# Optimization experiments

Measured on AMD Instinct MI355X. Metric: run time of the kernel, lower is better.

Reference implementation:

```python
import jax, jax.numpy as jnp
import numpy as np
import math

# ---- static config (mirrors init_kwargs) ----
B, CIN, COUT = 8, 32, 32
H, W = 256, 256
RADIUS_CUTOFF = 0.03
NR, NPHI = 6, 7               # kernel_shape = [6, 7] (anisotropic basis)
K = (NR - 1) * NPHI + 1       # 36 basis functions
EPS = 1e-5                    # InstanceNorm2d eps
NEG_SLOPE = 0.2


def _disco_psi(nh, nw, r_cutoff, nr, nphi):
    """Local DISCO filter basis on an equidistant [-1,1]^2 grid.
    Returns psi [K, P, P] (float32) and half-width p (P = 2p+1).
    Piecewise-linear hat functions in radius (nr rings incl. center) times
    hat functions in angle (nphi sectors), normalized and quadrature-weighted."""
    dy = 2.0 / nh
    dx = 2.0 / nw
    p = int(math.floor(r_cutoff / min(dx, dy)))
    off_y = (np.arange(-p, p + 1) * dy)[:, None]
    off_x = (np.arange(-p, p + 1) * dx)[None, :]
    r = np.sqrt(off_x ** 2 + off_y ** 2)                 # [P, P]
    phi = np.arctan2(off_y + 0 * off_x, off_x + 0 * off_y) % (2.0 * np.pi)
    dr = r_cutoff / nr
    dphi = 2.0 * np.pi / nphi
    ker = (nr - 1) * nphi + 1
    ik = np.arange(ker)[:, None, None]                   # [K,1,1]
    ir = ((ik - 1) // nphi + 1) * dr                     # ik=0 -> ring at r=0
    iphi = ((ik - 1) % nphi) * dphi
    norm = np.pi * (r_cutoff * nr / (nr + 1)) ** 2       # 2d normalization
    rv = np.clip(1.0 - np.abs(r[None] - ir) / dr, 0.0, None) * (r[None] <= r_cutoff)
    dphi_abs = np.abs(phi[None] - iphi)
    dphi_min = np.minimum(dphi_abs, 2.0 * np.pi - dphi_abs)
    pv = np.where(ik > 0, np.clip(1.0 - dphi_min / dphi, 0.0, None), 1.0)
    q = dx * dy                                          # quadrature weight
    psi = (rv * pv) * (q / norm)
    return jnp.asarray(psi, jnp.float32), p


def _upsample2x_bilinear_align_corners(x):
    """torch nn.Upsample(scale_factor=2, mode='bilinear', align_corners=True)."""
    b, c, hi, wi = x.shape
    ho, wo = 2 * hi, 2 * wi
    ys = jnp.linspace(0.0, hi - 1.0, ho)
    y0 = jnp.clip(jnp.floor(ys), 0, hi - 2).astype(jnp.int32)
    wy = (ys - y0.astype(ys.dtype))[None, None, :, None]
    x = x[:, :, y0, :] * (1.0 - wy) + x[:, :, y0 + 1, :] * wy
    xs = jnp.linspace(0.0, wi - 1.0, wo)
    x0 = jnp.clip(jnp.floor(xs), 0, wi - 2).astype(jnp.int32)
    wx = (xs - x0.astype(xs.dtype))[None, None, None, :]
    return x[:, :, :, x0] * (1.0 - wx) + x[:, :, :, x0 + 1] * wx


def setup_inputs() -> dict:
    key = jax.random.key(0)
    k1, k2 = jax.random.split(key)
    image = jax.random.normal(k1, (B, CIN, H, W), dtype=jnp.float32)
    # DISCO learnable weights: [out_ch, in_ch, kernel_size]
    scale = 1.0 / np.sqrt(CIN * K)
    weight = jax.random.normal(k2, (COUT, CIN, K), dtype=jnp.float32) * scale
    return {"image": image, "weight": weight}


def reference(image, weight):
    x = _upsample2x_bilinear_align_corners(image)
    # 2) equidistant DISCO conv: assemble dense kernel from basis, strided conv back to (H,W)
    psi, p = _disco_psi(2 * H, 2 * W, RADIUS_CUTOFF / 2.0, NR, NPHI)   # [K,P,P]
    kernel = jnp.einsum("oik,kyx->oiyx", weight, psi)                   # [O,I,P,P]
    y = jax.lax.conv_general_dilated(
        x, kernel, window_strides=(2, 2), padding=[(p, p), (p, p)],
        dimension_numbers=("NCHW", "OIHW", "NCHW"))                     # [B,O,H,W]
    # 3) InstanceNorm2d (no affine), biased variance over spatial dims
    mean = jnp.mean(y, axis=(2, 3), keepdims=True)
    var = jnp.var(y, axis=(2, 3), keepdims=True)
    y = (y - mean) * jax.lax.rsqrt(var + EPS)
    # 4) LeakyReLU(0.2)
    return jnp.where(y >= 0, y, NEG_SLOPE * y)
```

## Files before the change

kernel.cpp:

```cpp
#include <hip/hip_runtime.h>
#include <hip/hip_bf16.h>
#include <math.h>

#define B_     8
#define CIN_   32
#define COUT_  32
#define H_     256
#define W_     256
#define K_     36
#define P_     3
#define KW_    7
#define TAPS_  49
#define EPS_   1e-5f
#define SLOPE_ 0.2f

#define PART_OFF_F   28672
#define MEANRS_OFF_F 159744

#define IMG_PLANE_B   6736
#define IMG_ROW_B     336

#define XP_ROW   304
#define XO_BASE  11248

using short8_t  = __attribute__((ext_vector_type(8)))  short;
using f32x16_t  = __attribute__((ext_vector_type(16))) float;
using f32x4_t   = __attribute__((ext_vector_type(4)))  float;

__device__ inline ushort f32_to_bf16(float f) {
    unsigned int bits = __float_as_uint(f);
    unsigned int r = (bits + 0x7FFFu + ((bits >> 16) & 1u)) >> 16;
    return (ushort)r;
}

__global__ __launch_bounds__(256)
void build_kernel(const float* __restrict__ weight, ushort* __restrict__ kerB) {
    __shared__ float psi_s[2][K_];
    const int f  = blockIdx.x;
    const int p  = f & 3;
    const int ky = (f >> 2) % 7;
    const int oc = f / 28;
    const int tid = threadIdx.x;

    if (tid < 2 * K_) {
        const int tt = tid / K_;
        const int k  = tid - tt * K_;
        const int kx = 2 * p + tt;
        float val = 0.f;
        if (kx <= 6) {
            const double dxy   = 2.0 / 512.0;
            const double rcut  = 0.015;
            const int    nr    = 6, nphi = 7;
            const double dr    = rcut / nr;
            const double dphi  = 2.0 * M_PI / nphi;
            const double norm  = M_PI * (rcut * nr / (nr + 1)) * (rcut * nr / (nr + 1));
            const double q     = dxy * dxy;
            const double offy = (double)(ky - P_) * dxy;
            const double offx = (double)(kx - P_) * dxy;
            const double r    = sqrt(offx * offx + offy * offy);
            double phi = atan2(offy, offx);
            if (phi < 0.0) phi += 2.0 * M_PI;
            double ir, iphi;
            if (k == 0) { ir = 0.0; iphi = 0.0; }
            else        { ir = (double)((k - 1) / nphi + 1) * dr;
                          iphi = (double)((k - 1) % nphi) * dphi; }
            double rv = 1.0 - fabs(r - ir) / dr;
            rv = rv > 0.0 ? rv : 0.0;
            if (r > rcut) rv = 0.0;
            double pv = 1.0;
            if (k > 0) {
                double da = fabs(phi - iphi);
                double dm = da < (2.0 * M_PI - da) ? da : (2.0 * M_PI - da);
                pv = 1.0 - dm / dphi;
                pv = pv > 0.0 ? pv : 0.0;
            }
            val = (float)(rv * pv * q / norm);
        }
        psi_s[tt][k] = val;
    }
    __syncthreads();

    for (int e = tid; e < 512; e += 256) {
        const int lane = e >> 3;
        const int j    = e & 7;
        const int gs   = lane >> 5;
        const int n    = lane & 31;
        const int kx   = 2 * p + gs;
        float s = 0.f;
        if (kx <= 6) {
            const int ci = oc * 8 + j;
            const float* w = weight + (size_t)(n * CIN_ + ci) * K_;
            #pragma unroll
            for (int k = 0; k < K_; ++k) s = fmaf(w[k], psi_s[gs][k], s);
        }
        kerB[((size_t)f * 64 + lane) * 8 + j] = f32_to_bf16(s);
    }
}

__global__ __launch_bounds__(512, 8)
void conv_mfma(const float* __restrict__ image,
               const ushort* __restrict__ kerB,
               float* __restrict__ out,
               float* __restrict__ partials) {
    __shared__ float  Img_s[3368];
    __shared__ ushort Xup_s[11248];
    __shared__ float  wp[8][32][2];

    const int tid  = threadIdx.x;
    const int lane = tid & 63;
    const int w    = tid >> 6;
    const int j0 = blockIdx.x * 16;
    const int i0 = blockIdx.y * 16;
    const int b  = blockIdx.z;

    const int u0 = 2 * i0 - 3;
    const int v0 = 2 * j0 - 3;
    const int R0 = i0 - 2;
    const int C0 = j0 - 2;

    const int gs  = lane >> 5;
    const int tio = (lane & 31) >> 4;
    const int tj  = lane & 15;
    const int yb0 = 4 * w + 2 * tio;

    f32x16_t acc;
    #pragma unroll
    for (int q = 0; q < 16; ++q) acc[q] = 0.f;

    char* img_bytes = (char*)Img_s;
    char* xup_bytes = (char*)Xup_s;

    const float* imgb = image + (size_t)(b * CIN_) * (H_ * W_);

    for (int oc = 0; oc < 4; ++oc) {
        const float* img = imgb + (size_t)(oc * 8) * (H_ * W_);
        for (int e = tid; e < 800; e += 512) {
            const int p  = (e >= 400) ? 1 : 0;
            const int yx = e - p * 400;
            const int py = yx / 20, px = yx - py * 20;
            const int row = R0 + py, col = C0 + px;
            f32x4_t g = {0.f, 0.f, 0.f, 0.f};
            if ((unsigned)row < 256u && (unsigned)col < 256u) {
                const float* q = img + (size_t)p * 4 * (H_ * W_) + row * W_ + col;
                g[0] = q[0];
                g[1] = q[H_ * W_];
                g[2] = q[2 * (H_ * W_)];
                g[3] = q[3 * (H_ * W_)];
            }
            *(f32x4_t*)(img_bytes + p * IMG_PLANE_B + (py * 21 + px) * 16) = g;
        }
        __syncthreads();

        for (int e = tid; e < 703; e += 512) {
            const int y   = e / 19;
            const int xp  = e - 19 * y;
            const int x   = 2 * xp;
            const int ry  = y >> 1;
            const float wy =
                (float)((((y & 1) ? 510 : 255)) - (R0 + ry)) * (1.0f / 511.0f);
            const int Ax = C0 + xp;
            const float wx0 = (float)(255 - Ax) * (1.0f / 511.0f);
            const float wx1 = (float)(510 - Ax) * (1.0f / 511.0f);
            const bool oky = ((unsigned)(u0 + y) < 512u);
            const bool ok0 = oky && ((unsigned)(v0 + x) < 512u);
            const bool ok1 = oky && ((unsigned)(v0 + x + 1) < 512u) && (xp < 18);

            const char* lo = img_bytes + (ry * 21 + xp) * 16;
            const char* hi = lo + IMG_PLANE_B;
            const f32x4_t a00 = *(const f32x4_t*)(lo);
            const f32x4_t a01 = *(const f32x4_t*)(lo + 16);
            const f32x4_t a10 = *(const f32x4_t*)(lo + IMG_ROW_B);
            const f32x4_t a11 = *(const f32x4_t*)(lo + IMG_ROW_B + 16);
            const f32x4_t b00 = *(const f32x4_t*)(hi);
            const f32x4_t b01 = *(const f32x4_t*)(hi + 16);
            const f32x4_t b10 = *(const f32x4_t*)(hi + IMG_ROW_B);
            const f32x4_t b11 = *(const f32x4_t*)(hi + IMG_ROW_B + 16);

            const f32x4_t cA0 = a00 + wy * (a10 - a00);
            const f32x4_t cA1 = a01 + wy * (a11 - a01);
            const f32x4_t cB0 = b00 + wy * (b10 - b00);
            const f32x4_t cB1 = b01 + wy * (b11 - b01);

            {
                const f32x4_t va = cA0 + wx0 * (cA1 - cA0);
                const f32x4_t vb = cB0 + wx0 * (cB1 - cB0);
                __hip_bfloat162 h0 = __float22bfloat162_rn(make_float2(va[0], va[1]));
                __hip_bfloat162 h1 = __float22bfloat162_rn(make_float2(va[2], va[3]));
                __hip_bfloat162 h2 = __float22bfloat162_rn(make_float2(vb[0], vb[1]));
                __hip_bfloat162 h3 = __float22bfloat162_rn(make_float2(vb[2], vb[3]));
                union { short8_t s8; uint4 u4; } pk;
                pk.u4.x = ok0 ? *(unsigned int*)&h0 : 0u;
                pk.u4.y = ok0 ? *(unsigned int*)&h1 : 0u;
                pk.u4.z = ok0 ? *(unsigned int*)&h2 : 0u;
                pk.u4.w = ok0 ? *(unsigned int*)&h3 : 0u;
                *(short8_t*)(xup_bytes + y * XP_ROW + xp * 16) = pk.s8;
            }
            {
                const f32x4_t va = cA0 + wx1 * (cA1 - cA0);
                const f32x4_t vb = cB0 + wx1 * (cB1 - cB0);
                __hip_bfloat162 h0 = __float22bfloat162_rn(make_float2(va[0], va[1]));
                __hip_bfloat162 h1 = __float22bfloat162_rn(make_float2(va[2], va[3]));
                __hip_bfloat162 h2 = __float22bfloat162_rn(make_float2(vb[0], vb[1]));
                __hip_bfloat162 h3 = __float22bfloat162_rn(make_float2(vb[2], vb[3]));
                union { short8_t s8; uint4 u4; } pk;
                pk.u4.x = ok1 ? *(unsigned int*)&h0 : 0u;
                pk.u4.y = ok1 ? *(unsigned int*)&h1 : 0u;
                pk.u4.z = ok1 ? *(unsigned int*)&h2 : 0u;
                pk.u4.w = ok1 ? *(unsigned int*)&h3 : 0u;
                *(short8_t*)(xup_bytes + XO_BASE + y * XP_ROW + xp * 16) = pk.s8;
            }
        }
        __syncthreads();

        const int pbase = (gs ? XO_BASE : 0) + tj * 16;
        const ushort* kbp = kerB + ((size_t)(oc * 28) * 64 + lane) * 8;
        #pragma unroll
        for (int ky = 0; ky < KW_; ++ky) {
            short8_t bf[4];
            #pragma unroll
            for (int p = 0; p < 4; ++p)
                bf[p] = *(const short8_t*)(kbp + (size_t)(ky * 4 + p) * 512);
            const int rbase = pbase + (yb0 + ky) * XP_ROW;
            #pragma unroll
            for (int p = 0; p < 4; ++p) {
                const short8_t afrag = *(const short8_t*)(xup_bytes + rbase + p * 16);
                acc = __builtin_amdgcn_mfma_f32_32x32x16_bf16(afrag, bf[p], acc, 0, 0, 0);
            }
        }
        __syncthreads();
    }

    const int n = lane & 31;
    float* op = out + (size_t)(b * COUT_ + n) * (H_ * W_);
    const int ibase = i0 + 2 * w;
    #pragma unroll
    for (int grp = 0; grp < 4; ++grp) {
        const int ti  = ibase + (grp >> 1);
        const int tjj = j0 + ((grp & 1) ? 8 : 0) + 4 * gs;
        f32x4_t s;
        s[0] = acc[grp * 4 + 0]; s[1] = acc[grp * 4 + 1];
        s[2] = acc[grp * 4 + 2]; s[3] = acc[grp * 4 + 3];
        *(f32x4_t*)(op + (size_t)ti * W_ + tjj) = s;
    }

    float s1 = 0.f, s2 = 0.f;
    #pragma unroll
    for (int q = 0; q < 16; ++q) { s1 += acc[q]; s2 = fmaf(acc[q], acc[q], s2); }
    s1 += __shfl_xor(s1, 32);
    s2 += __shfl_xor(s2, 32);
    if (lane < 32) { wp[w][lane][0] = s1; wp[w][lane][1] = s2; }
    __syncthreads();
    if (tid < 32) {
        float t1 = 0.f, t2 = 0.f;
        #pragma unroll
        for (int wv = 0; wv < 8; ++wv) { t1 += wp[wv][tid][0]; t2 += wp[wv][tid][1]; }
        const int tile = blockIdx.y * 16 + blockIdx.x;
        float2* pp = (float2*)partials;
        pp[((b * 32 + tid) << 8) | tile] = make_float2(t1, t2);
    }
}

__global__ __launch_bounds__(64)
void stats_kernel(const float* __restrict__ partials, float* __restrict__ meanrs) {
    const int bo = blockIdx.x;
    const int l  = threadIdx.x;
    const float2* pp = (const float2*)partials + ((size_t)bo << 8);
    float s1 = 0.f, s2 = 0.f;
    #pragma unroll
    for (int k = 0; k < 4; ++k) {
        const float2 p = pp[l + 64 * k];
        s1 += p.x; s2 += p.y;
    }
    #pragma unroll
    for (int off = 32; off > 0; off >>= 1) {
        s1 += __shfl_down(s1, off);
        s2 += __shfl_down(s2, off);
    }
    if (l == 0) {
        const float inv = 1.0f / 65536.0f;
        const float m   = s1 * inv;
        const float var = s2 * inv - m * m;
        ((float2*)meanrs)[bo] = make_float2(m, 1.0f / sqrtf(var + EPS_));
    }
}

__global__ __launch_bounds__(256)
void norm2_kernel(float* __restrict__ y, const float* __restrict__ meanrs) {
    const int blk = blockIdx.x;
    const int bo  = blk >> 6;
    const float2 mr = ((const float2*)meanrs)[bo];
    const float m  = mr.x;
    const float rs = mr.y;

    const int e = blk * 256 + threadIdx.x;
    float4 v = ((const float4*)y)[e];
    v.x = (v.x - m) * rs; v.x = v.x >= 0.f ? v.x : SLOPE_ * v.x;
    v.y = (v.y - m) * rs; v.y = v.y >= 0.f ? v.y : SLOPE_ * v.y;
    v.z = (v.z - m) * rs; v.z = v.z >= 0.f ? v.z : SLOPE_ * v.z;
    v.w = (v.w - m) * rs; v.w = v.w >= 0.f ? v.w : SLOPE_ * v.w;
    ((float4*)y)[e] = v;
}

extern "C" void kernel_launch(void* const* d_in, const int* in_sizes, int n_in,
                              void* d_out, int out_size, void* d_ws, size_t ws_size,
                              hipStream_t stream) {
    const float* image  = (const float*)d_in[0];
    const float* weight = (const float*)d_in[1];
    float*  out      = (float*)d_out;
    ushort* kerB     = (ushort*)d_ws;
    float*  partials = (float*)d_ws + PART_OFF_F;
    float*  meanrs   = (float*)d_ws + MEANRS_OFF_F;

    build_kernel<<<dim3(112), dim3(256), 0, stream>>>(weight, kerB);
    conv_mfma<<<dim3(16, 16, B_), dim3(512), 0, stream>>>(image, kerB, out, partials);
    stats_kernel<<<dim3(256), dim3(64), 0, stream>>>(partials, meanrs);
    norm2_kernel<<<dim3(16384), dim3(256), 0, stream>>>(out, meanrs);
}
```

Baseline: 122.6 us.

## Pack conv taps in flat pairs to cut padded MFMA work

The 49 filter taps are now grouped into 25 flat tap pairs instead of 7 rows of 4 column pairs, where each row had one zero-padded slot. This lowers the MFMA count per channel group from 28 to 25. The weight-packing kernel and the A-fragment addressing are changed to match, and the LDS row pitch is widened so each pair's fragment can be addressed across rows, with a special case for the final half-empty pair. The cost is a larger shared-memory footprint, which may reduce occupancy, plus more complex address arithmetic.

```diff
diff --git a/kernel.cpp b/kernel.cpp
--- a/kernel.cpp
+++ b/kernel.cpp
@@ -11,17 +11,18 @@
 #define P_     3
 #define KW_    7
 #define TAPS_  49
+#define NPAIR_ 25
 #define EPS_   1e-5f
 #define SLOPE_ 0.2f
 
-#define PART_OFF_F   28672
-#define MEANRS_OFF_F 159744
+#define PART_OFF_F   25600
+#define MEANRS_OFF_F 156672
 
 #define IMG_PLANE_B   6736
 #define IMG_ROW_B     336
 
-#define XP_ROW   304
-#define XO_BASE  11248
+#define XP_ROW   336
+#define XO_BASE  12480
 
 using short8_t  = __attribute__((ext_vector_type(8)))  short;
 using f32x16_t  = __attribute__((ext_vector_type(16))) float;
@@ -37,17 +38,18 @@
 void build_kernel(const float* __restrict__ weight, ushort* __restrict__ kerB) {
     __shared__ float psi_s[2][K_];
     const int f  = blockIdx.x;
-    const int p  = f & 3;
-    const int ky = (f >> 2) % 7;
-    const int oc = f / 28;
+    const int i  = f % NPAIR_;
+    const int oc = f / NPAIR_;
     const int tid = threadIdx.x;
 
     if (tid < 2 * K_) {
         const int tt = tid / K_;
         const int k  = tid - tt * K_;
-        const int kx = 2 * p + tt;
+        const int tap = 2 * i + tt;
         float val = 0.f;
-        if (kx <= 6) {
+        if (tap <= 48) {
+            const int ky = tap / 7;
+            const int kx = tap % 7;
             const double dxy   = 2.0 / 512.0;
             const double rcut  = 0.015;
             const int    nr    = 6, nphi = 7;
@@ -85,9 +87,9 @@
         const int j    = e & 7;
         const int gs   = lane >> 5;
         const int n    = lane & 31;
-        const int kx   = 2 * p + gs;
+        const int tap  = 2 * i + gs;
         float s = 0.f;
-        if (kx <= 6) {
+        if (tap <= 48) {
             const int ci = oc * 8 + j;
             const float* w = weight + (size_t)(n * CIN_ + ci) * K_;
             #pragma unroll
@@ -103,7 +105,7 @@
                float* __restrict__ out,
                float* __restrict__ partials) {
     __shared__ float  Img_s[3368];
-    __shared__ ushort Xup_s[11248];
+    __shared__ ushort Xup_s[12456];
     __shared__ float  wp[8][32][2];
 
     const int tid  = threadIdx.x;
@@ -212,19 +214,32 @@
         }
         __syncthreads();
 
-        const int pbase = (gs ? XO_BASE : 0) + tj * 16;
-        const ushort* kbp = kerB + ((size_t)(oc * 28) * 64 + lane) * 8;
+        const int abase = yb0 * XP_ROW + tj * 16;
+        const ushort* kbp = kerB + ((size_t)(oc * NPAIR_) * 64 + lane) * 8;
+        short8_t bf[5];
         #pragma unroll
-        for (int ky = 0; ky < KW_; ++ky) {
-            short8_t bf[4];
+        for (int gq = 0; gq < 5; ++gq) {
             #pragma unroll
-            for (int p = 0; p < 4; ++p)
-                bf[p] = *(const short8_t*)(kbp + (size_t)(ky * 4 + p) * 512);
-            const int rbase = pbase + (yb0 + ky) * XP_ROW;
+            for (int u = 0; u < 5; ++u)
+                bf[u] = *(const short8_t*)(kbp + (size_t)((gq * 5 + u) * 512));
             #pragma unroll
-            for (int p = 0; p < 4; ++p) {
-                const short8_t afrag = *(const short8_t*)(xup_bytes + rbase + p * 16);
-                acc = __builtin_amdgcn_mfma_f32_32x32x16_bf16(afrag, bf[p], acc, 0, 0, 0);
+            for (int u = 0; u < 5; ++u) {
+                const int i = gq * 5 + u;
+                int addr;
+                if (i < 24) {
+                    const int t0 = 2 * i, t1 = 2 * i + 1;
+                    const int c0 = (t0 / 7) * XP_ROW + ((t0 % 7) & 1 ? XO_BASE : 0)
+                                 + ((t0 % 7) >> 1) * 16;
+                    const int c1 = (t1 / 7) * XP_ROW + ((t1 % 7) & 1 ? XO_BASE : 0)
+                                 + ((t1 % 7) >> 1) * 16;
+                    addr = abase + (gs ? c1 : c0);
+                } else {
+                    const int c0 = 6 * XP_ROW + 3 * 16;
+                    addr = gs ? (XO_BASE + yb0 * XP_ROW + 18 * 16)
+                              : (abase + c0);
+                }
+                const short8_t afrag = *(const short8_t*)(xup_bytes + addr);
+                acc = __builtin_amdgcn_mfma_f32_32x32x16_bf16(afrag, bf[u], acc, 0, 0, 0);
             }
         }
         __syncthreads();
@@ -311,7 +326,7 @@
     float*  partials = (float*)d_ws + PART_OFF_F;
     float*  meanrs   = (float*)d_ws + MEANRS_OFF_F;
 
-    build_kernel<<<dim3(112), dim3(256), 0, stream>>>(weight, kerB);
+    build_kernel<<<dim3(4 * NPAIR_), dim3(256), 0, stream>>>(weight, kerB);
     conv_mfma<<<dim3(16, 16, B_), dim3(512), 0, stream>>>(image, kerB, out, partials);
     stats_kernel<<<dim3(256), dim3(64), 0, stream>>>(partials, meanrs);
     norm2_kernel<<<dim3(16384), dim3(256), 0, stream>>>(out, meanrs);
```

Result: slower. 158.3 us (+29.1%).

## Repack 7x7 conv taps into 25 bf16 MFMA pairs to drop padded taps

Applied to the files above, without the earlier changes.

Before, each kernel row's seven taps were packed into four MFMA K-slices, one of which was half zero padding, for 28 MFMAs per channel group. Now the first six columns of each row form three pairs, and the last column across rows is paired vertically. This gives 25 MFMAs per channel group and cuts wasted matrix work and weight loads. It needs an extra zeroed shared-memory row, a larger Xup buffer and changed workspace offsets. The A-fragment addressing for the column pairs must line up exactly with the even/odd plane layout.

```diff
diff --git a/kernel.cpp b/kernel.cpp
--- a/kernel.cpp
+++ b/kernel.cpp
@@ -11,17 +11,18 @@
 #define P_     3
 #define KW_    7
 #define TAPS_  49
+#define NPAIR_ 25
 #define EPS_   1e-5f
 #define SLOPE_ 0.2f
 
-#define PART_OFF_F   28672
-#define MEANRS_OFF_F 159744
+#define PART_OFF_F   25600
+#define MEANRS_OFF_F 156672
 
 #define IMG_PLANE_B   6736
 #define IMG_ROW_B     336
 
 #define XP_ROW   304
-#define XO_BASE  11248
+#define XO_BASE  11552
 
 using short8_t  = __attribute__((ext_vector_type(8)))  short;
 using f32x16_t  = __attribute__((ext_vector_type(16))) float;
@@ -33,21 +34,31 @@
     return (ushort)r;
 }
 
+__host__ __device__ inline int pair_tap(int pi, int tt) {
+    if (pi < 21) {
+        const int ky = pi / 3, c = pi % 3;
+        return ky * 7 + 2 * c + tt;
+    }
+    const int row = 2 * (pi - 21) + tt;
+    return (row <= 6) ? (row * 7 + 6) : -1;
+}
+
 __global__ __launch_bounds__(256)
 void build_kernel(const float* __restrict__ weight, ushort* __restrict__ kerB) {
     __shared__ float psi_s[2][K_];
     const int f  = blockIdx.x;
-    const int p  = f & 3;
-    const int ky = (f >> 2) % 7;
-    const int oc = f / 28;
+    const int pi = f % NPAIR_;
+    const int oc = f / NPAIR_;
     const int tid = threadIdx.x;
 
     if (tid < 2 * K_) {
         const int tt = tid / K_;
         const int k  = tid - tt * K_;
-        const int kx = 2 * p + tt;
+        const int tap = pair_tap(pi, tt);
         float val = 0.f;
-        if (kx <= 6) {
+        if (tap >= 0) {
+            const int ky = tap / 7;
+            const int kx = tap % 7;
             const double dxy   = 2.0 / 512.0;
             const double rcut  = 0.015;
             const int    nr    = 6, nphi = 7;
@@ -85,9 +96,8 @@
         const int j    = e & 7;
         const int gs   = lane >> 5;
         const int n    = lane & 31;
-        const int kx   = 2 * p + gs;
         float s = 0.f;
-        if (kx <= 6) {
+        if (pair_tap(pi, gs) >= 0) {
             const int ci = oc * 8 + j;
             const float* w = weight + (size_t)(n * CIN_ + ci) * K_;
             #pragma unroll
@@ -103,7 +113,7 @@
                float* __restrict__ out,
                float* __restrict__ partials) {
     __shared__ float  Img_s[3368];
-    __shared__ ushort Xup_s[11248];
+    __shared__ ushort Xup_s[11552];
     __shared__ float  wp[8][32][2];
 
     const int tid  = threadIdx.x;
@@ -129,6 +139,11 @@
 
     char* img_bytes = (char*)Img_s;
     char* xup_bytes = (char*)Xup_s;
+
+    if (tid < 19) {
+        const short8_t z = {0,0,0,0,0,0,0,0};
+        *(short8_t*)(xup_bytes + 37 * XP_ROW + tid * 16) = z;
+    }
 
     const float* imgb = image + (size_t)(b * CIN_) * (H_ * W_);
 
@@ -212,20 +227,30 @@
         }
         __syncthreads();
 
-        const int pbase = (gs ? XO_BASE : 0) + tj * 16;
-        const ushort* kbp = kerB + ((size_t)(oc * 28) * 64 + lane) * 8;
+        const ushort* kbp = kerB + ((size_t)(oc * NPAIR_) * 64 + lane) * 8;
+        const int baseA = (gs ? XO_BASE : 0) + yb0 * XP_ROW + tj * 16;
+        const int baseB = (yb0 + gs) * XP_ROW + (tj + 3) * 16;
+
         #pragma unroll
         for (int ky = 0; ky < KW_; ++ky) {
-            short8_t bf[4];
-            #pragma unroll
-            for (int p = 0; p < 4; ++p)
-                bf[p] = *(const short8_t*)(kbp + (size_t)(ky * 4 + p) * 512);
-            const int rbase = pbase + (yb0 + ky) * XP_ROW;
-            #pragma unroll
-            for (int p = 0; p < 4; ++p) {
-                const short8_t afrag = *(const short8_t*)(xup_bytes + rbase + p * 16);
-                acc = __builtin_amdgcn_mfma_f32_32x32x16_bf16(afrag, bf[p], acc, 0, 0, 0);
-            }
+            short8_t bf0 = *(const short8_t*)(kbp + (size_t)((ky * 3 + 0) * 512));
+            short8_t bf1 = *(const short8_t*)(kbp + (size_t)((ky * 3 + 1) * 512));
+            short8_t bf2 = *(const short8_t*)(kbp + (size_t)((ky * 3 + 2) * 512));
+            const int rbase = baseA + ky * XP_ROW;
+            const short8_t a0 = *(const short8_t*)(xup_bytes + rbase);
+            acc = __builtin_amdgcn_mfma_f32_32x32x16_bf16(a0, bf0, acc, 0, 0, 0);
+            const short8_t a1 = *(const short8_t*)(xup_bytes + rbase + 16);
+            acc = __builtin_amdgcn_mfma_f32_32x32x16_bf16(a1, bf1, acc, 0, 0, 0);
+            const short8_t a2 = *(const short8_t*)(xup_bytes + rbase + 32);
+            acc = __builtin_amdgcn_mfma_f32_32x32x16_bf16(a2, bf2, acc, 0, 0, 0);
+        }
+        #pragma unroll
+        for (int q = 0; q < 4; ++q) {
+            const short8_t bfq =
+                *(const short8_t*)(kbp + (size_t)((21 + q) * 512));
+            const short8_t aq =
+                *(const short8_t*)(xup_bytes + baseB + q * (2 * XP_ROW));
+            acc = __builtin_amdgcn_mfma_f32_32x32x16_bf16(aq, bfq, acc, 0, 0, 0);
         }
         __syncthreads();
     }
@@ -311,7 +336,7 @@
     float*  partials = (float*)d_ws + PART_OFF_F;
     float*  meanrs   = (float*)d_ws + MEANRS_OFF_F;
 
-    build_kernel<<<dim3(112), dim3(256), 0, stream>>>(weight, kerB);
+    build_kernel<<<dim3(4 * NPAIR_), dim3(256), 0, stream>>>(weight, kerB);
     conv_mfma<<<dim3(16, 16, B_), dim3(512), 0, stream>>>(image, kerB, out, partials);
     stats_kernel<<<dim3(256), dim3(64), 0, stream>>>(partials, meanrs);
     norm2_kernel<<<dim3(16384), dim3(256), 0, stream>>>(out, meanrs);
```

After: 116.8 us, median of 2. -4.8%, faster.
